# Kernel optimization log

Measured on AMD Instinct MI355X. Metric: run time of the kernel, lower is better.

Reference implementation:

```python
import jax, jax.numpy as jnp
import numpy as np

SDE_SIGMA_MIN = 0.01   # VE-SDE sigma(0)
SDE_SIGMA_MAX = 100.0  # VE-SDE sigma(1)
SIGMA_MIN = 1e-4       # model's sigma_min regularizer


def sde_sigma(t):
    # Variance-exploding SDE noise schedule: geometric interpolation.
    return SDE_SIGMA_MIN * (SDE_SIGMA_MAX / SDE_SIGMA_MIN) ** t


def setup_inputs() -> dict:
    key = jax.random.key(0)
    k1, k2, k3 = jax.random.split(key, 3)
    B, N, D = 4096, 8192, 256
    t = jax.random.uniform(k1, (B,), dtype=jnp.float32)          # diffusion times in [0,1)
    x = jax.random.normal(k2, (B, D), dtype=jnp.float32)         # query points
    samples = jax.random.normal(k3, (N, D), dtype=jnp.float32)   # dataset samples
    return {"t": t, "x": x, "samples": samples}


def reference(t, x, samples):
    # t: [B], x: [B, D], samples: [N, D]
    t_scale = sde_sigma(t)                                  # [B]
    denom = (t_scale ** 2 + SIGMA_MIN ** 2)[:, None]        # [B, 1]
    # ||s_i - x_b||^2 via expansion (avoids materializing [B, N, D])
    s2 = jnp.sum(samples ** 2, axis=-1)                     # [N]
    x2 = jnp.sum(x ** 2, axis=-1, keepdims=True)            # [B, 1]
    d2 = x2 - 2.0 * (x @ samples.T) + s2[None, :]           # [B, N]
    # W_i = exp(-0.5 d2 / denom); max-subtract + normalize == stable softmax
    W = jax.nn.softmax(-0.5 * d2 / denom, axis=-1)          # [B, N]
    mean_s = W @ samples                                    # [B, D]
    # t_scale * sum_i W_i (s_i - x) / denom, with sum_i W_i == 1
    return t_scale[:, None] * (mean_s - x) / denom
```

## Files before the change

### kernel.cpp

```cpp
#include <hip/hip_runtime.h>
#include <math.h>


typedef float  f32x4 __attribute__((ext_vector_type(4)));
typedef short  s16x8 __attribute__((ext_vector_type(8)));
typedef unsigned int u32x4 __attribute__((ext_vector_type(4)));
typedef unsigned short u16;

#define LOG2E   1.44269504088896f
#define L2_10K  13.2877123795494f
#define L2_001 -6.64385618977472f
#define SMIN2   1e-8f
#define DDIM    256
#define DEFER_THR 12.0f

#if defined(__has_builtin)
#if __has_builtin(__builtin_amdgcn_exp2f)
#define EXP2(x) __builtin_amdgcn_exp2f(x)
#endif
#endif
#ifndef EXP2
#define EXP2(x) exp2f(x)
#endif

#define GL16(gp, lp) \
  __builtin_amdgcn_global_load_lds( \
      (const __attribute__((address_space(1))) unsigned int*)(gp), \
      (__attribute__((address_space(3))) unsigned int*)(lp), 16, 0, 0)

__device__ __forceinline__ u16 bf16_rne(float f) {
  unsigned int u = __builtin_bit_cast(unsigned int, f);
  u = (u + 0x7FFFu + ((u >> 16) & 1u)) >> 16;
  return (u16)u;
}
__device__ __forceinline__ float bf16_to_f(u16 h) {
  unsigned int u = ((unsigned int)h) << 16;
  return __builtin_bit_cast(float, u);
}
__device__ __forceinline__ float f16_to_f(u16 h) {
  int s = (h >> 15) & 1, e = (h >> 10) & 31, m = h & 1023;
  float v;
  if (e == 0)       v = ldexpf((float)m, -24);
  else if (e == 31) v = 3.0e38f;
  else              v = ldexpf((float)(1024 + m), e - 25);
  return s ? -v : v;
}

__device__ __forceinline__ int classify_t_dtype(const void* tp) {
  const u16*          u16p = (const u16*)tp;
  const unsigned int* u32p = (const unsigned int*)tp;
  int c16 = 0, c32 = 0;
  for (int i = 0; i < 128; ++i) {
    u16 u = u16p[i];
    int e = (u >> 7) & 0xFF;
    if (!(u & 0x8000) && e >= 113 && e <= 126) c16++;
  }
  for (int i = 0; i < 64; ++i) {
    unsigned int w = u32p[i];
    int e = (int)((w >> 23) & 0xFF);
    if (!(w & 0x80000000u) && e >= 113 && e <= 126) c32++;
  }
  if (c32 >= 51) return (c16 >= 102) ? 0 : 1;
  return 2;
}
__device__ __forceinline__ float load_t(const void* tp, int i, int mode) {
  float v;
  if (mode == 0)      v = bf16_to_f(((const u16*)tp)[i]);
  else if (mode == 1) v = ((const float*)tp)[i];
  else                v = f16_to_f(((const u16*)tp)[i]);
  return fminf(fmaxf(v, 0.f), 1.f);
}

__global__ __launch_bounds__(256)
void prep_all(const float* __restrict__ smp, const void* __restrict__ t,
              u16* __restrict__ gkhi, u16* __restrict__ gklo,
              float* __restrict__ gs2, u16* __restrict__ gvt,
              int* __restrict__ tflag, int N)
{
  int nb_rows = N >> 2;
  if ((int)blockIdx.x < nb_rows) {
    if (blockIdx.x == 0 && threadIdx.x == 0) *tflag = classify_t_dtype(t);
    int row  = blockIdx.x * 4 + (threadIdx.x >> 6);
    int lane = threadIdx.x & 63;
    float4 v4 = *(const float4*)(smp + (size_t)row * DDIM + lane * 4);
    float v[4] = {v4.x, v4.y, v4.z, v4.w};
    ushort4 h, l;
    u16 hh[4], ll[4];
    float s2 = 0.f;
#pragma unroll
    for (int e = 0; e < 4; ++e) {
      hh[e] = bf16_rne(v[e]);
      ll[e] = bf16_rne(v[e] - bf16_to_f(hh[e]));
      s2 = fmaf(v[e], v[e], s2);
    }
    h.x = hh[0]; h.y = hh[1]; h.z = hh[2]; h.w = hh[3];
    l.x = ll[0]; l.y = ll[1]; l.z = ll[2]; l.w = ll[3];
    int ci  = lane >> 1;
    int col = (((ci ^ (row & 7)) << 3) | ((lane & 1) << 2));
    *(ushort4*)(gkhi + (size_t)row * DDIM + col) = h;
    *(ushort4*)(gklo + (size_t)row * DDIM + col) = l;
#pragma unroll
    for (int msk = 1; msk <= 32; msk <<= 1) s2 += __shfl_xor(s2, msk);
    if (lane == 0) gs2[row] = 0.5f * s2;
  } else {
    int bt = blockIdx.x - nb_rows;
    int d  = threadIdx.x;
    int n0 = bt * 32;
    u16 buf[32];
#pragma unroll
    for (int i = 0; i < 32; ++i)
      buf[i] = bf16_rne(smp[(size_t)(n0 + i) * DDIM + d]);
    u16* dst = gvt + ((size_t)bt * 256 + d) * 32;
    int vkey = (d >> 1) & 3;
#pragma unroll
    for (int c = 0; c < 4; ++c)
      *(s16x8*)(dst + ((c ^ vkey) << 3)) = *(s16x8*)&buf[c * 8];
  }
}


struct __align__(16) Smem {
  u16 khi[32 * 256];
  u16 klo[32 * 256];
  u16 vt [2][256 * 32];
};

__global__ __launch_bounds__(256, 2)
void flash_kernel(const void* __restrict__ t, const float* __restrict__ x,
                  const u16* __restrict__ gkhi, const u16* __restrict__ gklo,
                  const u16* __restrict__ gvt, const float* __restrict__ gs2,
                  const int* __restrict__ tflag, float* __restrict__ out,
                  float* __restrict__ pO, float* __restrict__ pm,
                  float* __restrict__ pl, int B, int N)
{
  __shared__ Smem sm;
  const int tid  = threadIdx.x;
  const int wave = tid >> 6, lane = tid & 63;
  const int lq = lane >> 4, lr = lane & 15;
  const int m0 = blockIdx.x * 64 + wave * 16;
  const int nsplit = gridDim.y, split = blockIdx.y;
  const int tiles_total = N >> 5;
  const int tq = tiles_total / nsplit, tr = tiles_total % nsplit;
  const int tile0 = split * tq + (split < tr ? split : tr);
  const int iters = tq + (split < tr ? 1 : 0);
  const int n0b = tile0 << 5;
  const int tmode = *tflag;

  float invd;
  {
    float tv = load_t(t, m0 + lr, tmode);
    float ts = EXP2(fmaf(tv, L2_10K, L2_001));
    invd = LOG2E / (ts * ts + SMIN2);
  }

  s16x8 qhi[8], qlo[8];
  {
    const float* xr = x + (size_t)(m0 + lr) * DDIM;
#pragma unroll
    for (int ks = 0; ks < 8; ++ks) {
      const float4* p4 = (const float4*)(xr + ks * 32 + lq * 8);
      float4 a = p4[0], b = p4[1];
      float v[8] = {a.x, a.y, a.z, a.w, b.x, b.y, b.z, b.w};
#pragma unroll
      for (int j = 0; j < 8; ++j) {
        u16 h = bf16_rne(v[j]);
        u16 l = bf16_rne(v[j] - bf16_to_f(h));
        qhi[ks][j] = (short)h;
        qlo[ks][j] = (short)l;
      }
    }
  }

  f32x4 O[16];
#pragma unroll
  for (int dt = 0; dt < 16; ++dt) O[dt] = (f32x4){0.f, 0.f, 0.f, 0.f};
  float mrun = -1e30f, lrun = 0.f;

  const int krsw = lr & 7;
  const int wo = (wave << 12) + lane * 16;
  const int lq4 = lq << 2;

  {
    size_t tb = (size_t)n0b << 9;
    const char* gk = (const char*)gkhi + tb + wo;
    const char* gl = (const char*)gklo + tb + wo;
    const char* gv = (const char*)gvt  + tb + wo;
    char* lk = (char*)sm.khi   + (wave << 12);
    char* ll = (char*)sm.klo   + (wave << 12);
    char* lv = (char*)sm.vt[0] + (wave << 12);
    GL16(gk,        lk);        GL16(gk + 1024, lk + 1024);
    GL16(gk + 2048, lk + 2048); GL16(gk + 3072, lk + 3072);
    GL16(gl,        ll);        GL16(gl + 1024, ll + 1024);
    GL16(gl + 2048, ll + 2048); GL16(gl + 3072, ll + 3072);
    GL16(gv,        lv);        GL16(gv + 1024, lv + 1024);
    GL16(gv + 2048, lv + 2048); GL16(gv + 3072, lv + 3072);
  }

  int n0 = n0b, cur = 0;
  for (int it = 0; it < iters; ++it) {
    __syncthreads();

    float4 s2a4 = *(const float4*)(gs2 + n0 + lq4);
    float4 s2b4 = *(const float4*)(gs2 + n0 + 16 + lq4);

    f32x4 acc[2];
    acc[0] = (f32x4){0.f, 0.f, 0.f, 0.f};
    acc[1] = (f32x4){0.f, 0.f, 0.f, 0.f};
    __builtin_amdgcn_s_setprio(1);
#pragma unroll
    for (int nt = 0; nt < 2; ++nt) {
#pragma unroll
      for (int ks = 0; ks < 8; ++ks) {
        int co = (((ks << 2) + lq) ^ krsw) << 3;
        const s16x8 bh = *(const s16x8*)&sm.khi[(nt * 16 + lr) * 256 + co];
        const s16x8 bl = *(const s16x8*)&sm.klo[(nt * 16 + lr) * 256 + co];
        acc[nt] = __builtin_amdgcn_mfma_f32_16x16x32_bf16(bh, qhi[ks], acc[nt], 0, 0, 0);
        acc[nt] = __builtin_amdgcn_mfma_f32_16x16x32_bf16(bh, qlo[ks], acc[nt], 0, 0, 0);
        acc[nt] = __builtin_amdgcn_mfma_f32_16x16x32_bf16(bl, qhi[ks], acc[nt], 0, 0, 0);
      }
    }
    __builtin_amdgcn_s_setprio(0);

    __syncthreads();

    if (it + 1 < iters) {
      size_t tb = (size_t)(n0 + 32) << 9;
      const char* gk = (const char*)gkhi + tb + wo;
      const char* gl = (const char*)gklo + tb + wo;
      const char* gv = (const char*)gvt  + tb + wo;
      char* lk = (char*)sm.khi + (wave << 12);
      char* ll = (char*)sm.klo + (wave << 12);
      char* lv = (char*)sm.vt[cur ^ 1] + (wave << 12);
      GL16(gk,        lk);        GL16(gk + 1024, lk + 1024);
      GL16(gk + 2048, lk + 2048); GL16(gk + 3072, lk + 3072);
      GL16(gl,        ll);        GL16(gl + 1024, ll + 1024);
      GL16(gl + 2048, ll + 2048); GL16(gl + 3072, ll + 3072);
      GL16(gv,        lv);        GL16(gv + 1024, lv + 1024);
      GL16(gv + 2048, lv + 2048); GL16(gv + 3072, lv + 3072);
    }

    float L0[4], L1[4];
    float tmax = -1e30f;
#pragma unroll
    for (int r = 0; r < 4; ++r) {
      L0[r] = (acc[0][r] - s2a4[r]) * invd;
      L1[r] = (acc[1][r] - s2b4[r]) * invd;
      tmax = fmaxf(tmax, fmaxf(L0[r], L1[r]));
    }
    tmax = fmaxf(tmax, __shfl_xor(tmax, 16));
    tmax = fmaxf(tmax, __shfl_xor(tmax, 32));
    float mnew = mrun;
    if (!__all(tmax - mnew <= DEFER_THR)) {
      mnew = fmaxf(mrun, tmax);
      float alpha = EXP2(mrun - mnew);
      mrun = mnew;
      lrun *= alpha;
      float a0 = __shfl(alpha, lq4 + 0), a1 = __shfl(alpha, lq4 + 1);
      float a2 = __shfl(alpha, lq4 + 2), a3 = __shfl(alpha, lq4 + 3);
#pragma unroll
      for (int dt = 0; dt < 16; ++dt) {
        O[dt][0] *= a0; O[dt][1] *= a1; O[dt][2] *= a2; O[dt][3] *= a3;
      }
    }
    u16 p0[4], p1[4];
    float ps = 0.f;
#pragma unroll
    for (int r = 0; r < 4; ++r) {
      p0[r] = bf16_rne(EXP2(L0[r] - mnew));
      p1[r] = bf16_rne(EXP2(L1[r] - mnew));
      ps += bf16_to_f(p0[r]) + bf16_to_f(p1[r]);
    }
    ps += __shfl_xor(ps, 16);
    ps += __shfl_xor(ps, 32);
    lrun += ps;

    s16x8 pa;
    {
      unsigned A0 = (unsigned)p0[0] | ((unsigned)p0[1] << 16);
      unsigned A1 = (unsigned)p0[2] | ((unsigned)p0[3] << 16);
      unsigned B0 = (unsigned)p1[0] | ((unsigned)p1[1] << 16);
      unsigned B1 = (unsigned)p1[2] | ((unsigned)p1[3] << 16);
      int s0 = ((lq & 1) << 5) + lr;
      int s1 = s0 + 16;
      unsigned xa0 = (unsigned)__shfl((int)A0, s0);
      unsigned xa1 = (unsigned)__shfl((int)A1, s0);
      unsigned xa2 = (unsigned)__shfl((int)A0, s1);
      unsigned xa3 = (unsigned)__shfl((int)A1, s1);
      unsigned xb0 = (unsigned)__shfl((int)B0, s0);
      unsigned xb1 = (unsigned)__shfl((int)B1, s0);
      unsigned xb2 = (unsigned)__shfl((int)B0, s1);
      unsigned xb3 = (unsigned)__shfl((int)B1, s1);
      u32x4 pw;
      pw.x = (lq < 2) ? xa0 : xb0;
      pw.y = (lq < 2) ? xa1 : xb1;
      pw.z = (lq < 2) ? xa2 : xb2;
      pw.w = (lq < 2) ? xa3 : xb3;
      pa = __builtin_bit_cast(s16x8, pw);
    }

    {
      const u16* vtc = sm.vt[cur];
      __builtin_amdgcn_s_setprio(1);
#pragma unroll
      for (int dt = 0; dt < 16; ++dt) {
        int row = dt * 16 + lr;
        const s16x8 bv = *(const s16x8*)&vtc[(row << 5) + ((lq ^ ((row >> 1) & 3)) << 3)];
        O[dt] = __builtin_amdgcn_mfma_f32_16x16x32_bf16(pa, bv, O[dt], 0, 0, 0);
      }
      __builtin_amdgcn_s_setprio(0);
    }
    cur ^= 1;
    n0 += 32;
  }

  if (nsplit == 1) {
    float inv = 1.f / lrun;
    float il0 = __shfl(inv, lq4 + 0), il1 = __shfl(inv, lq4 + 1);
    float il2 = __shfl(inv, lq4 + 2), il3 = __shfl(inv, lq4 + 3);
    float il[4] = {il0, il1, il2, il3};
#pragma unroll
    for (int r = 0; r < 4; ++r) {
      int gm = m0 + lq4 + r;
      float tv = load_t(t, gm, tmode);
      float ts = EXP2(fmaf(tv, L2_10K, L2_001));
      float den = ts * ts + SMIN2;
      float sc = ts / den;
#pragma unroll
      for (int dt = 0; dt < 16; ++dt) {
        int d = dt * 16 + lr;
        out[(size_t)gm * DDIM + d] = sc * (O[dt][r] * il[r] - x[(size_t)gm * DDIM + d]);
      }
    }
  } else {
    size_t obase = (size_t)split * B * DDIM;
#pragma unroll
    for (int r = 0; r < 4; ++r) {
      int gm = m0 + lq4 + r;
#pragma unroll
      for (int dt = 0; dt < 16; ++dt)
        pO[obase + (size_t)gm * DDIM + dt * 16 + lr] = O[dt][r];
    }
    if (lane < 16) {
      pm[(size_t)split * B + m0 + lane] = mrun;
      pl[(size_t)split * B + m0 + lane] = lrun;
    }
  }
}

__global__ __launch_bounds__(256)
void combine_kernel(const void* __restrict__ t, const float* __restrict__ x,
                    const float* __restrict__ pO, const float* __restrict__ pm,
                    const float* __restrict__ pl, float* __restrict__ out,
                    const int* __restrict__ tflag, int nsplit, int B)
{
  int idx = blockIdx.x * 256 + threadIdx.x;
  int b = idx >> 6;
  const int tmode = *tflag;
  float M = -1e30f;
  for (int s = 0; s < nsplit; ++s) M = fmaxf(M, pm[(size_t)s * B + b]);
  float4 num = {0.f, 0.f, 0.f, 0.f};
  float den = 0.f;
  for (int s = 0; s < nsplit; ++s) {
    float w = EXP2(pm[(size_t)s * B + b] - M);
    float4 po = ((const float4*)pO)[(size_t)s * B * 64 + idx];
    num.x += w * po.x; num.y += w * po.y; num.z += w * po.z; num.w += w * po.w;
    den += w * pl[(size_t)s * B + b];
  }
  float il = 1.f / den;
  float tv = load_t(t, b, tmode);
  float ts = EXP2(fmaf(tv, L2_10K, L2_001));
  float sc = ts / (ts * ts + SMIN2);
  float4 xx = ((const float4*)x)[idx];
  float4 o;
  o.x = sc * (num.x * il - xx.x);
  o.y = sc * (num.y * il - xx.y);
  o.z = sc * (num.z * il - xx.z);
  o.w = sc * (num.w * il - xx.w);
  ((float4*)out)[idx] = o;
}

extern "C" void kernel_launch(void* const* d_in, const int* in_sizes, int n_in,
                              void* d_out, int out_size, void* d_ws, size_t ws_size,
                              hipStream_t stream) {
  int xi = 0, si = 0, ti = 0;
  for (int i = 0; i < 3; ++i) {
    if (in_sizes[i] == out_size) xi = i;
    if (in_sizes[i] > in_sizes[si]) si = i;
    if (in_sizes[i] < in_sizes[ti]) ti = i;
  }
  const void*  t   = d_in[ti];
  const float* x   = (const float*)d_in[xi];
  const float* smp = (const float*)d_in[si];
  float* out = (float*)d_out;
  int B = out_size / DDIM;
  int N = in_sizes[si] / DDIM;

  size_t plane = (size_t)N * DDIM;
  u16*   gkhi = (u16*)d_ws;
  u16*   gklo = gkhi + plane;
  u16*   gvt  = gklo + plane;
  float* gs2  = (float*)(gvt + plane);
  int*   tflag = (int*)(gs2 + N);
  float* pO   = gs2 + N + 4;
  size_t fixed = plane * 6 + (size_t)N * 4 + 16;
  size_t per = (size_t)B * DDIM * sizeof(float) + (size_t)B * 2 * sizeof(float);

  const int cand[4] = {8, 4, 2, 1};
  int ns = 1;
  for (int i = 0; i < 4; ++i)
    if (fixed + (size_t)cand[i] * per <= ws_size) { ns = cand[i]; break; }
  float* pm = pO + (size_t)ns * B * DDIM;
  float* pl = pm + (size_t)ns * B;

  prep_all<<<dim3(N / 4 + N / 32), 256, 0, stream>>>(smp, t, gkhi, gklo, gs2,
                                                     gvt, tflag, N);
  flash_kernel<<<dim3(B / 64, ns), 256, 0, stream>>>(t, x, gkhi, gklo, gvt, gs2, tflag,
                                                     out, pO, pm, pl, B, N);
  if (ns > 1)
    combine_kernel<<<dim3(B * 64 / 256), 256, 0, stream>>>(t, x, pO, pm, pl, out, tflag, ns, B);
}
```

Measured before the change: 167.6 us.

## Software-pipeline the PV MFMA one tile behind the softmax with triple-buffered V

New measurement: 176.2 us. 5.1% more time.

```diff
diff --git a/kernel.cpp b/kernel.cpp
--- a/kernel.cpp
+++ b/kernel.cpp
@@ -122,7 +122,7 @@
 struct __align__(16) Smem {
   u16 khi[32 * 256];
   u16 klo[32 * 256];
-  u16 vt [2][256 * 32];
+  u16 vt [3][256 * 32];
 };
 
 __global__ __launch_bounds__(256, 2)
@@ -196,9 +196,30 @@
     GL16(gv + 2048, lv + 2048); GL16(gv + 3072, lv + 3072);
   }
 
-  int n0 = n0b, cur = 0;
+  s16x8 pa_prev = {0, 0, 0, 0, 0, 0, 0, 0};
+  s16x8 bvp[8];
+
+  int n0 = n0b;
   for (int it = 0; it < iters; ++it) {
+    const int sp = (it + 2) % 3;
+    const int sn = (it + 1) % 3;
+
+    if (it > 0) {
+#pragma unroll
+      for (int dt = 0; dt < 8; ++dt) {
+        int row = dt * 16 + lr;
+        bvp[dt] = *(const s16x8*)&sm.vt[sp][(row << 5) + ((lq ^ ((row >> 1) & 3)) << 3)];
+      }
+    }
+
     __syncthreads();
+
+    if (it + 1 < iters) {
+      const char* gv = (const char*)gvt + ((size_t)(n0 + 32) << 9) + wo;
+      char* lv = (char*)sm.vt[sn] + (wave << 12);
+      GL16(gv,        lv);        GL16(gv + 1024, lv + 1024);
+      GL16(gv + 2048, lv + 2048); GL16(gv + 3072, lv + 3072);
+    }
 
     float4 s2a4 = *(const float4*)(gs2 + n0 + lq4);
     float4 s2b4 = *(const float4*)(gs2 + n0 + 16 + lq4);
@@ -227,55 +248,65 @@
       size_t tb = (size_t)(n0 + 32) << 9;
       const char* gk = (const char*)gkhi + tb + wo;
       const char* gl = (const char*)gklo + tb + wo;
-      const char* gv = (const char*)gvt  + tb + wo;
       char* lk = (char*)sm.khi + (wave << 12);
       char* ll = (char*)sm.klo + (wave << 12);
-      char* lv = (char*)sm.vt[cur ^ 1] + (wave << 12);
       GL16(gk,        lk);        GL16(gk + 1024, lk + 1024);
       GL16(gk + 2048, lk + 2048); GL16(gk + 3072, lk + 3072);
       GL16(gl,        ll);        GL16(gl + 1024, ll + 1024);
       GL16(gl + 2048, ll + 2048); GL16(gl + 3072, ll + 3072);
-      GL16(gv,        lv);        GL16(gv + 1024, lv + 1024);
-      GL16(gv + 2048, lv + 2048); GL16(gv + 3072, lv + 3072);
-    }
-
-    float L0[4], L1[4];
-    float tmax = -1e30f;
-#pragma unroll
-    for (int r = 0; r < 4; ++r) {
-      L0[r] = (acc[0][r] - s2a4[r]) * invd;
-      L1[r] = (acc[1][r] - s2b4[r]) * invd;
-      tmax = fmaxf(tmax, fmaxf(L0[r], L1[r]));
-    }
-    tmax = fmaxf(tmax, __shfl_xor(tmax, 16));
-    tmax = fmaxf(tmax, __shfl_xor(tmax, 32));
-    float mnew = mrun;
-    if (!__all(tmax - mnew <= DEFER_THR)) {
-      mnew = fmaxf(mrun, tmax);
-      float alpha = EXP2(mrun - mnew);
-      mrun = mnew;
-      lrun *= alpha;
-      float a0 = __shfl(alpha, lq4 + 0), a1 = __shfl(alpha, lq4 + 1);
-      float a2 = __shfl(alpha, lq4 + 2), a3 = __shfl(alpha, lq4 + 3);
-#pragma unroll
-      for (int dt = 0; dt < 16; ++dt) {
-        O[dt][0] *= a0; O[dt][1] *= a1; O[dt][2] *= a2; O[dt][3] *= a3;
-      }
-    }
-    u16 p0[4], p1[4];
-    float ps = 0.f;
-#pragma unroll
-    for (int r = 0; r < 4; ++r) {
-      p0[r] = bf16_rne(EXP2(L0[r] - mnew));
-      p1[r] = bf16_rne(EXP2(L1[r] - mnew));
-      ps += bf16_to_f(p0[r]) + bf16_to_f(p1[r]);
-    }
-    ps += __shfl_xor(ps, 16);
-    ps += __shfl_xor(ps, 32);
-    lrun += ps;
-
-    s16x8 pa;
+    }
+
+    if (it > 0) {
+      const u16* vtp = sm.vt[sp];
+      __builtin_amdgcn_s_setprio(1);
+#pragma unroll
+      for (int dt = 0; dt < 8; ++dt)
+        O[dt] = __builtin_amdgcn_mfma_f32_16x16x32_bf16(pa_prev, bvp[dt], O[dt], 0, 0, 0);
+#pragma unroll
+      for (int dt = 8; dt < 16; ++dt) {
+        int row = dt * 16 + lr;
+        const s16x8 bv = *(const s16x8*)&vtp[(row << 5) + ((lq ^ ((row >> 1) & 3)) << 3)];
+        O[dt] = __builtin_amdgcn_mfma_f32_16x16x32_bf16(pa_prev, bv, O[dt], 0, 0, 0);
+      }
+      __builtin_amdgcn_s_setprio(0);
+    }
+
     {
+      float L0[4], L1[4];
+      float tmax = -1e30f;
+#pragma unroll
+      for (int r = 0; r < 4; ++r) {
+        L0[r] = (acc[0][r] - s2a4[r]) * invd;
+        L1[r] = (acc[1][r] - s2b4[r]) * invd;
+        tmax = fmaxf(tmax, fmaxf(L0[r], L1[r]));
+      }
+      tmax = fmaxf(tmax, __shfl_xor(tmax, 16));
+      tmax = fmaxf(tmax, __shfl_xor(tmax, 32));
+      float mnew = mrun;
+      if (!__all(tmax - mnew <= DEFER_THR)) {
+        mnew = fmaxf(mrun, tmax);
+        float alpha = EXP2(mrun - mnew);
+        mrun = mnew;
+        lrun *= alpha;
+        float a0 = __shfl(alpha, lq4 + 0), a1 = __shfl(alpha, lq4 + 1);
+        float a2 = __shfl(alpha, lq4 + 2), a3 = __shfl(alpha, lq4 + 3);
+#pragma unroll
+        for (int dt = 0; dt < 16; ++dt) {
+          O[dt][0] *= a0; O[dt][1] *= a1; O[dt][2] *= a2; O[dt][3] *= a3;
+        }
+      }
+      u16 p0[4], p1[4];
+      float ps = 0.f;
+#pragma unroll
+      for (int r = 0; r < 4; ++r) {
+        p0[r] = bf16_rne(EXP2(L0[r] - mnew));
+        p1[r] = bf16_rne(EXP2(L1[r] - mnew));
+        ps += bf16_to_f(p0[r]) + bf16_to_f(p1[r]);
+      }
+      ps += __shfl_xor(ps, 16);
+      ps += __shfl_xor(ps, 32);
+      lrun += ps;
+
       unsigned A0 = (unsigned)p0[0] | ((unsigned)p0[1] << 16);
       unsigned A1 = (unsigned)p0[2] | ((unsigned)p0[3] << 16);
       unsigned B0 = (unsigned)p1[0] | ((unsigned)p1[1] << 16);
@@ -295,22 +326,20 @@
       pw.y = (lq < 2) ? xa1 : xb1;
       pw.z = (lq < 2) ? xa2 : xb2;
       pw.w = (lq < 2) ? xa3 : xb3;
-      pa = __builtin_bit_cast(s16x8, pw);
-    }
-
-    {
-      const u16* vtc = sm.vt[cur];
-      __builtin_amdgcn_s_setprio(1);
-#pragma unroll
-      for (int dt = 0; dt < 16; ++dt) {
-        int row = dt * 16 + lr;
-        const s16x8 bv = *(const s16x8*)&vtc[(row << 5) + ((lq ^ ((row >> 1) & 3)) << 3)];
-        O[dt] = __builtin_amdgcn_mfma_f32_16x16x32_bf16(pa, bv, O[dt], 0, 0, 0);
-      }
-      __builtin_amdgcn_s_setprio(0);
-    }
-    cur ^= 1;
+      pa_prev = __builtin_bit_cast(s16x8, pw);
+    }
     n0 += 32;
+  }
+
+  {
+    const int sl = (iters + 2) % 3;
+    const u16* vtp = sm.vt[sl];
+#pragma unroll
+    for (int dt = 0; dt < 16; ++dt) {
+      int row = dt * 16 + lr;
+      const s16x8 bv = *(const s16x8*)&vtp[(row << 5) + ((lq ^ ((row >> 1) & 3)) << 3)];
+      O[dt] = __builtin_amdgcn_mfma_f32_16x16x32_bf16(pa_prev, bv, O[dt], 0, 0, 0);
+    }
   }
 
   if (nsplit == 1) {
```

## Fuse split-K combine into flash kernel via last-block atomic counter

Applied to the files above, without the earlier changes.

Measured after the change: 305.3 us. +82.1%, slower.

```diff
diff --git a/kernel.cpp b/kernel.cpp
--- a/kernel.cpp
+++ b/kernel.cpp
@@ -75,11 +75,13 @@
 void prep_all(const float* __restrict__ smp, const void* __restrict__ t,
               u16* __restrict__ gkhi, u16* __restrict__ gklo,
               float* __restrict__ gs2, u16* __restrict__ gvt,
-              int* __restrict__ tflag, int N)
+              int* __restrict__ tflag, int* __restrict__ flags,
+              int nflags, int N)
 {
   int nb_rows = N >> 2;
   if ((int)blockIdx.x < nb_rows) {
     if (blockIdx.x == 0 && threadIdx.x == 0) *tflag = classify_t_dtype(t);
+    if (blockIdx.x == 0 && (int)threadIdx.x < nflags) flags[threadIdx.x] = 0;
     int row  = blockIdx.x * 4 + (threadIdx.x >> 6);
     int lane = threadIdx.x & 63;
     float4 v4 = *(const float4*)(smp + (size_t)row * DDIM + lane * 4);
@@ -131,9 +133,11 @@
                   const u16* __restrict__ gvt, const float* __restrict__ gs2,
                   const int* __restrict__ tflag, float* __restrict__ out,
                   float* __restrict__ pO, float* __restrict__ pm,
-                  float* __restrict__ pl, int B, int N)
+                  float* __restrict__ pl, int* __restrict__ flags,
+                  int B, int N)
 {
   __shared__ Smem sm;
+  __shared__ int sOld;
   const int tid  = threadIdx.x;
   const int wave = tid >> 6, lane = tid & 63;
   const int lq = lane >> 4, lr = lane & 15;
@@ -344,39 +348,41 @@
       pm[(size_t)split * B + m0 + lane] = mrun;
       pl[(size_t)split * B + m0 + lane] = lrun;
     }
-  }
-}
-
-__global__ __launch_bounds__(256)
-void combine_kernel(const void* __restrict__ t, const float* __restrict__ x,
-                    const float* __restrict__ pO, const float* __restrict__ pm,
-                    const float* __restrict__ pl, float* __restrict__ out,
-                    const int* __restrict__ tflag, int nsplit, int B)
-{
-  int idx = blockIdx.x * 256 + threadIdx.x;
-  int b = idx >> 6;
-  const int tmode = *tflag;
-  float M = -1e30f;
-  for (int s = 0; s < nsplit; ++s) M = fmaxf(M, pm[(size_t)s * B + b]);
-  float4 num = {0.f, 0.f, 0.f, 0.f};
-  float den = 0.f;
-  for (int s = 0; s < nsplit; ++s) {
-    float w = EXP2(pm[(size_t)s * B + b] - M);
-    float4 po = ((const float4*)pO)[(size_t)s * B * 64 + idx];
-    num.x += w * po.x; num.y += w * po.y; num.z += w * po.z; num.w += w * po.w;
-    den += w * pl[(size_t)s * B + b];
-  }
-  float il = 1.f / den;
-  float tv = load_t(t, b, tmode);
-  float ts = EXP2(fmaf(tv, L2_10K, L2_001));
-  float sc = ts / (ts * ts + SMIN2);
-  float4 xx = ((const float4*)x)[idx];
-  float4 o;
-  o.x = sc * (num.x * il - xx.x);
-  o.y = sc * (num.y * il - xx.y);
-  o.z = sc * (num.z * il - xx.z);
-  o.w = sc * (num.w * il - xx.w);
-  ((float4*)out)[idx] = o;
+
+    __threadfence();
+    __syncthreads();
+    if (tid == 0) sOld = atomicAdd(&flags[blockIdx.x], 1);
+    __syncthreads();
+    if (sOld == nsplit - 1) {
+      __threadfence();
+      for (int k = tid; k < 64 * 64; k += 256) {
+        int b   = blockIdx.x * 64 + (k >> 6);
+        int idx = (b << 6) + (k & 63);
+        float M = -1e30f;
+        for (int s = 0; s < nsplit; ++s) M = fmaxf(M, pm[(size_t)s * B + b]);
+        float4 num = {0.f, 0.f, 0.f, 0.f};
+        float den = 0.f;
+        for (int s = 0; s < nsplit; ++s) {
+          float w = EXP2(pm[(size_t)s * B + b] - M);
+          float4 po = ((const float4*)pO)[(size_t)s * B * 64 + idx];
+          num.x += w * po.x; num.y += w * po.y;
+          num.z += w * po.z; num.w += w * po.w;
+          den += w * pl[(size_t)s * B + b];
+        }
+        float ili = 1.f / den;
+        float tv = load_t(t, b, tmode);
+        float ts = EXP2(fmaf(tv, L2_10K, L2_001));
+        float sc = ts / (ts * ts + SMIN2);
+        float4 xx = ((const float4*)x)[idx];
+        float4 o;
+        o.x = sc * (num.x * ili - xx.x);
+        o.y = sc * (num.y * ili - xx.y);
+        o.z = sc * (num.z * ili - xx.z);
+        o.w = sc * (num.w * ili - xx.w);
+        ((float4*)out)[idx] = o;
+      }
+    }
+  }
 }
 
 extern "C" void kernel_launch(void* const* d_in, const int* in_sizes, int n_in,
@@ -394,6 +400,7 @@
   float* out = (float*)d_out;
   int B = out_size / DDIM;
   int N = in_sizes[si] / DDIM;
+  int ngrp = B / 64;
 
   size_t plane = (size_t)N * DDIM;
   u16*   gkhi = (u16*)d_ws;
@@ -402,7 +409,7 @@
   float* gs2  = (float*)(gvt + plane);
   int*   tflag = (int*)(gs2 + N);
   float* pO   = gs2 + N + 4;
-  size_t fixed = plane * 6 + (size_t)N * 4 + 16;
+  size_t fixed = plane * 6 + (size_t)N * 4 + 16 + (size_t)ngrp * 4;
   size_t per = (size_t)B * DDIM * sizeof(float) + (size_t)B * 2 * sizeof(float);
 
   const int cand[4] = {8, 4, 2, 1};
@@ -411,11 +418,10 @@
     if (fixed + (size_t)cand[i] * per <= ws_size) { ns = cand[i]; break; }
   float* pm = pO + (size_t)ns * B * DDIM;
   float* pl = pm + (size_t)ns * B;
+  int* flags = (int*)(pl + (size_t)ns * B);
 
   prep_all<<<dim3(N / 4 + N / 32), 256, 0, stream>>>(smp, t, gkhi, gklo, gs2,
-                                                     gvt, tflag, N);
+                                                     gvt, tflag, flags, ngrp, N);
   flash_kernel<<<dim3(B / 64, ns), 256, 0, stream>>>(t, x, gkhi, gklo, gvt, gs2, tflag,
-                                                     out, pO, pm, pl, B, N);
-  if (ns > 1)
-    combine_kernel<<<dim3(B * 64 / 256), 256, 0, stream>>>(t, x, pO, pm, pl, out, tflag, ns, B);
-}
+                                                     out, pO, pm, pl, flags, B, N);
+}
```
